# Kernel optimization log

Hardware: AMD Instinct MI355X
Metric: run time of the kernel (lower is better)

Reference implementation:

```python
import jax, jax.numpy as jnp
import numpy as np

H = 512; L = 2; V = 128; B = 128; T = 256; LW = 32; SOS = 1


def _lstm_scan(xs, Wih, Whh, b, reverse=False):
    # xs: [B, T, in]; Wih: [in, 4H]; Whh: [H, 4H]; b: [4H]
    Bq, Hh = xs.shape[0], Whh.shape[0]
    h0 = jnp.zeros((Bq, Hh), xs.dtype)

    def step(carry, xt):
        h, c = carry
        i, f, g, o = jnp.split(xt @ Wih + h @ Whh + b, 4, axis=-1)
        c = jax.nn.sigmoid(f) * c + jax.nn.sigmoid(i) * jnp.tanh(g)
        h = jax.nn.sigmoid(o) * jnp.tanh(c)
        return (h, c), h

    (hT, cT), ys = jax.lax.scan(step, (h0, h0), jnp.swapaxes(xs, 0, 1), reverse=reverse)
    return jnp.swapaxes(ys, 0, 1), hT, cT


def setup_inputs() -> dict:
    key = jax.random.key(0)
    ks = jax.random.split(key, 17)
    s = 0.05
    rn = lambda k, shape: jax.random.normal(k, shape, jnp.float32) * s
    return {
        'x': jax.random.normal(ks[0], (B, T, 2), jnp.float32),
        'enc_l0_Wih': rn(ks[1], (2, 2, 4 * H)),
        'enc_l0_Whh': rn(ks[2], (2, H, 4 * H)),
        'enc_l0_b': rn(ks[3], (2, 4 * H)),
        'enc_l1_Wih': rn(ks[4], (2, 2 * H, 4 * H)),
        'enc_l1_Whh': rn(ks[5], (2, H, 4 * H)),
        'enc_l1_b': rn(ks[6], (2, 4 * H)),
        'dec_Wih': rn(ks[7], (L, H, 4 * H)),
        'dec_Whh': rn(ks[8], (L, H, 4 * H)),
        'dec_b': rn(ks[9], (L, 4 * H)),
        'emb': rn(ks[10], (V, H)),
        'Wq': rn(ks[11], (H, 2 * H)),
        'bq': rn(ks[12], (2 * H,)),
        'Wc': rn(ks[13], (3 * H, H)),
        'bc': rn(ks[14], (H,)),
        'Wf': rn(ks[15], (H, V)),
        'bf': rn(ks[16], (V,)),
    }


def _forward(x, enc_l0_Wih, enc_l0_Whh, enc_l0_b, enc_l1_Wih, enc_l1_Whh, enc_l1_b,
             dec_Wih, dec_Whh, dec_b, emb, Wq, bq, Wc, bc, Wf, bf):
    # --- encoder: 2-layer bidirectional LSTM ---
    hs, cs = [], []
    inp = x
    for (Wih, Whh, b) in ((enc_l0_Wih, enc_l0_Whh, enc_l0_b),
                          (enc_l1_Wih, enc_l1_Whh, enc_l1_b)):
        yf, hf, cf = _lstm_scan(inp, Wih[0], Whh[0], b[0], reverse=False)
        yb, hb, cb = _lstm_scan(inp, Wih[1], Whh[1], b[1], reverse=True)
        inp = jnp.concatenate([yf, yb], axis=-1)
        hs.append(hf + hb)  # sum fwd+bwd final states (as in original)
        cs.append(cf + cb)
    enc_outs = inp                     # [B, T, 2H]
    h0 = jnp.stack(hs)                 # [L, B, H]
    c0 = jnp.stack(cs)
    tok0 = jnp.full((x.shape[0],), SOS, jnp.int32)

    def dec_step(carry, _):
        h, c, tok = carry
        layer_in = emb[tok]            # [B, H]
        nh, nc = [], []
        for l in range(L):
            i, f, g, o = jnp.split(layer_in @ dec_Wih[l] + h[l] @ dec_Whh[l] + dec_b[l], 4, axis=-1)
            cl = jax.nn.sigmoid(f) * c[l] + jax.nn.sigmoid(i) * jnp.tanh(g)
            hl = jax.nn.sigmoid(o) * jnp.tanh(cl)
            nh.append(hl); nc.append(cl)
            layer_in = hl
        dec_out = layer_in             # [B, H]
        query = dec_out @ Wq + bq      # [B, 2H]
        attn = jax.nn.softmax(jnp.einsum('bte,be->bt', enc_outs, query), axis=1)  # [B, T]
        context = jnp.einsum('bt,bte->be', attn, enc_outs)                        # [B, 2H]
        combined = jnp.concatenate([dec_out, context], axis=-1) @ Wc + bc         # [B, H]
        logits = combined @ Wf + bf                                                # [B, V]
        tok = jnp.argmax(logits, axis=-1).astype(jnp.int32)
        return (jnp.stack(nh), jnp.stack(nc), tok), (logits, attn)

    (hF, cF, _), (logits_seq, attn_seq) = jax.lax.scan(dec_step, (h0, c0, tok0), None, length=LW)
    output_seq = jnp.swapaxes(logits_seq, 0, 1)        # [B, LW, V]
    attention = jnp.transpose(attn_seq, (1, 2, 0))     # [B, T, LW]
    return output_seq, hF, cF, attention


def reference(x, enc_l0_Wih, enc_l0_Whh, enc_l0_b, enc_l1_Wih, enc_l1_Whh, enc_l1_b,
              dec_Wih, dec_Whh, dec_b, emb, Wq, bq, Wc, bc, Wf, bf):
    return _forward(x, enc_l0_Wih, enc_l0_Whh, enc_l0_b, enc_l1_Wih, enc_l1_Whh, enc_l1_b,
                    dec_Wih, dec_Whh, dec_b, emb, Wq, bq, Wc, bc, Wf, bf)
```

## Files before the change

kernel.cpp:

```cpp
#include <hip/hip_runtime.h>
#include <hip/hip_fp16.h>
#include <hip/hip_cooperative_groups.h>
#include <math.h>

#define NB 128
#define NT 256
#define NH 512
#define NG 2048
#define NV 128
#define NLW 32

__device__ __forceinline__ float sigf(float x){ return 1.0f/(1.0f + expf(-x)); }
__device__ __forceinline__ void fma4(float4& a, float s, float4 w){
  a.x += s*w.x; a.y += s*w.y; a.z += s*w.z; a.w += s*w.w;
}
__device__ __forceinline__ float4 ldh4(const __half* p){
  const __half2* p2 = (const __half2*)p;
  const float2 a = __half22float2(p2[0]);
  const float2 b = __half22float2(p2[1]);
  return make_float4(a.x, a.y, b.x, b.y);
}
__device__ __forceinline__ void ldh8(const __half* p, float4& lo, float4& hi){
  const float4 raw = *(const float4*)p;
  const __half2* h2 = (const __half2*)&raw;
  const float2 a = __half22float2(h2[0]);
  const float2 b = __half22float2(h2[1]);
  const float2 c = __half22float2(h2[2]);
  const float2 d = __half22float2(h2[3]);
  lo = make_float4(a.x, a.y, b.x, b.y);
  hi = make_float4(c.x, c.y, d.x, d.y);
}
__device__ __forceinline__ void dot4(float& acc, const float4 a, const float4 b){
  acc += a.x*b.x + a.y*b.y + a.z*b.z + a.w*b.w;
}

__device__ __forceinline__ void stc_f(float* p, float v){
  union { float f; unsigned u; } c; c.f = v;
  __hip_atomic_store((unsigned*)p, c.u, __ATOMIC_RELAXED, __HIP_MEMORY_SCOPE_AGENT);
}
__device__ __forceinline__ void stc_i(int* p, int v){
  __hip_atomic_store(p, v, __ATOMIC_RELAXED, __HIP_MEMORY_SCOPE_AGENT);
}

#define FBAR_FLAG0 1088
#define DBAR_FLAG0 1024

__device__ __forceinline__ void full_core(int* bar, int step) {
  const int g = blockIdx.x >> 4;
  const int prev = __hip_atomic_fetch_add(&bar[g*64], 1,
                     __ATOMIC_RELAXED, __HIP_MEMORY_SCOPE_AGENT);
  if (prev == 15) {
    const int r = __hip_atomic_fetch_add(&bar[16*64], 1,
                     __ATOMIC_RELAXED, __HIP_MEMORY_SCOPE_AGENT);
    if (r == 15) {
      #pragma unroll
      for (int i = 0; i < 16; ++i)
        __hip_atomic_store(&bar[i*64], 0, __ATOMIC_RELAXED, __HIP_MEMORY_SCOPE_AGENT);
      __hip_atomic_store(&bar[16*64], 0, __ATOMIC_RELAXED, __HIP_MEMORY_SCOPE_AGENT);
      asm volatile("s_waitcnt vmcnt(0)" ::: "memory");
      #pragma unroll 8
      for (int i = 0; i < 256; ++i)
        __hip_atomic_store(&bar[FBAR_FLAG0 + i*32], step,
                           __ATOMIC_RELAXED, __HIP_MEMORY_SCOPE_AGENT);
    }
  }
}
__device__ __forceinline__ void full_arrive(int* bar, int step) {
  __syncthreads();
  if (threadIdx.x == 0) {
    asm volatile("s_waitcnt vmcnt(0)" ::: "memory");
    full_core(bar, step);
  }
}
__device__ __forceinline__ void full_arrive_f(int* bar, int step) {
  __syncthreads();
  if (threadIdx.x == 0) {
    __threadfence();
    full_core(bar, step);
  }
}
__device__ __forceinline__ void full_wait(int* bar, int step) {
  if (threadIdx.x == 0) {
    int* my = &bar[FBAR_FLAG0 + blockIdx.x*32];
    while (__hip_atomic_load(my, __ATOMIC_RELAXED,
                             __HIP_MEMORY_SCOPE_AGENT) < step)
      __builtin_amdgcn_s_sleep(2);
    __threadfence();
  }
  __syncthreads();
}

__device__ __forceinline__ void dir_arrive(int* dbar, int step) {
  __syncthreads();
  if (threadIdx.x == 0) {
    asm volatile("s_waitcnt vmcnt(0)" ::: "memory");
    const int l = blockIdx.x & 127;
    const int g = l >> 4;
    const int prev = __hip_atomic_fetch_add(&dbar[g*64], 1,
                       __ATOMIC_RELAXED, __HIP_MEMORY_SCOPE_AGENT);
    if (prev == 15) {
      const int r = __hip_atomic_fetch_add(&dbar[8*64], 1,
                       __ATOMIC_RELAXED, __HIP_MEMORY_SCOPE_AGENT);
      if (r == 7) {
        #pragma unroll
        for (int i = 0; i < 8; ++i)
          __hip_atomic_store(&dbar[i*64], 0, __ATOMIC_RELAXED, __HIP_MEMORY_SCOPE_AGENT);
        __hip_atomic_store(&dbar[8*64], 0, __ATOMIC_RELAXED, __HIP_MEMORY_SCOPE_AGENT);
        asm volatile("s_waitcnt vmcnt(0)" ::: "memory");
        #pragma unroll 8
        for (int i = 0; i < 128; ++i)
          __hip_atomic_store(&dbar[DBAR_FLAG0 + i*32], step,
                             __ATOMIC_RELAXED, __HIP_MEMORY_SCOPE_AGENT);
      }
    }
  }
}
__device__ __forceinline__ void dir_wait(int* dbar, int step) {
  if (threadIdx.x == 0) {
    int* my = &dbar[DBAR_FLAG0 + (blockIdx.x & 127)*32];
    while (__hip_atomic_load(my, __ATOMIC_RELAXED,
                             __HIP_MEMORY_SCOPE_AGENT) < step)
      __builtin_amdgcn_s_sleep(2);
    __threadfence();
  }
  __syncthreads();
}

struct EncParams {
  const float* x;
  const float* W0ih; const float* W0hh; const float* b0;
  const float* W1ih; const float* W1hh; const float* b1;
  __half* y0; __half* enc;
  float* h0buf; float* h1buf;
  float* c0fin; float* c1fin;
  int*   bar;
};

#define W1T_ROW 1542
#define W0T_ROW 518
#define ENC_LDS_FLOATS (16*W1T_ROW + 16*W0T_ROW + 16 + 16 + 128*17)
#define ENC_LDS_BYTES  (ENC_LDS_FLOATS*4)

__device__ __forceinline__ void l1_ih_part(const __half* y0t, const float* W1T,
                                           const float* bias1, int bg2, int cg2,
                                           float acc[2][4]) {
  #pragma unroll
  for (int i = 0; i < 2; ++i)
    #pragma unroll
    for (int j = 0; j < 4; ++j)
      acc[i][j] = bias1[cg2*4 + j];
  const long r0 = (long)(bg2*2+0)*1024, r1 = (long)(bg2*2+1)*1024;
  #pragma unroll 2
  for (int k = 0; k < 1024; k += 8) {
    float4 a0lo, a0hi, a1lo, a1hi;
    ldh8(y0t + r0 + k, a0lo, a0hi);
    ldh8(y0t + r1 + k, a1lo, a1hi);
    #pragma unroll
    for (int j = 0; j < 4; ++j) {
      const float4 wlo = *(const float4*)&W1T[(cg2*4+j)*W1T_ROW + k];
      const float4 whi = *(const float4*)&W1T[(cg2*4+j)*W1T_ROW + k + 4];
      dot4(acc[0][j], a0lo, wlo); dot4(acc[0][j], a0hi, whi);
      dot4(acc[1][j], a1lo, wlo); dot4(acc[1][j], a1hi, whi);
    }
  }
}

__global__ __launch_bounds__(256, 1)
void encoder_kernel(EncParams P) {
  const int tid = threadIdx.x;
  const int bid = blockIdx.x;
  const int dir = bid >> 7;
  const int n0  = (bid & 127) * 4;
  int* dbar = P.bar + dir*8192;
  int* fbar = P.bar + 16384;

  extern __shared__ float lds[];
  float* W1T   = lds;
  float* W0T   = lds + 16*W1T_ROW;
  float* bias0 = W0T + 16*W0T_ROW;
  float* bias1 = bias0 + 16;
  float* gsm   = bias1 + 16;

  {
    const float* Wih1 = P.W1ih + (long)dir*1024*NG;
    const float* Whh1 = P.W1hh + (long)dir*512*NG;
    for (int e = tid; e < 16*1536; e += 256) {
      const int ci = e & 15, kk = e >> 4;
      const int gc = (ci>>2)*NH + n0 + (ci&3);
      W1T[ci*W1T_ROW + kk] = (kk < 1024) ? Wih1[(long)kk*NG + gc]
                                         : Whh1[(long)(kk-1024)*NG + gc];
    }
    const float* Wih0 = P.W0ih + (long)dir*2*NG;
    const float* Whh0 = P.W0hh + (long)dir*512*NG;
    for (int e = tid; e < 16*512; e += 256) {
      const int ci = e & 15, kk = e >> 4;
      const int gc = (ci>>2)*NH + n0 + (ci&3);
      W0T[ci*W0T_ROW + 4 + kk] = Whh0[(long)kk*NG + gc];
    }
    if (tid < 32) {
      const int ci = tid & 15, kk = tid >> 4;
      const int gc = (ci>>2)*NH + n0 + (ci&3);
      W0T[ci*W0T_ROW + kk] = Wih0[(long)kk*NG + gc];
    }
    if (tid < 16) {
      const int gc = (tid>>2)*NH + n0 + (tid&3);
      bias0[tid] = P.b0[(long)dir*NG + gc];
      bias1[tid] = P.b1[(long)dir*NG + gc];
    }
  }
  __syncthreads();

  int dstep = 0;
  float creg0 = 0.f, creg1 = 0.f;

  {
    const int bg1 = tid >> 3;
    const int cg1 = tid & 7;
    for (int p = 0; p < NT; ++p) {
      const int t = dir ? (NT-1 - p) : p;
      const float* hp = P.h0buf + (long)((p&1)*2 + dir)*65536;
      float acc[4][2];
      #pragma unroll
      for (int i = 0; i < 4; ++i) { acc[i][0] = bias0[cg1*2]; acc[i][1] = bias0[cg1*2+1]; }
      {
        const float w00 = W0T[(cg1*2+0)*W0T_ROW + 0], w01 = W0T[(cg1*2+0)*W0T_ROW + 1];
        const float w10 = W0T[(cg1*2+1)*W0T_ROW + 0], w11 = W0T[(cg1*2+1)*W0T_ROW + 1];
        #pragma unroll
        for (int i = 0; i < 4; ++i) {
          const int b = bg1*4 + i;
          const float x0 = P.x[(long)b*(NT*2) + t*2 + 0];
          const float x1 = P.x[(long)b*(NT*2) + t*2 + 1];
          acc[i][0] += x0*w00 + x1*w01;
          acc[i][1] += x0*w10 + x1*w11;
        }
      }
      #pragma unroll 4
      for (int k = 0; k < NH; k += 4) {
        const float4 w0 = *(const float4*)&W0T[(cg1*2+0)*W0T_ROW + 4 + k];
        const float4 w1 = *(const float4*)&W0T[(cg1*2+1)*W0T_ROW + 4 + k];
        #pragma unroll
        for (int i = 0; i < 4; ++i) {
          const float4 a = *(const float4*)&hp[(long)(bg1*4+i)*NH + k];
          dot4(acc[i][0], a, w0);
          dot4(acc[i][1], a, w1);
        }
      }
      #pragma unroll
      for (int i = 0; i < 4; ++i) {
        gsm[(bg1*4+i)*17 + cg1*2 + 0] = acc[i][0];
        gsm[(bg1*4+i)*17 + cg1*2 + 1] = acc[i][1];
      }
      __syncthreads();
      {
        float* hnext = P.h0buf + (long)(((p+1)&1)*2 + dir)*65536;
        #pragma unroll
        for (int r = 0; r < 2; ++r) {
          const int pi2 = tid + r*256;
          const int b = pi2 >> 2, nl = pi2 & 3;
          const float iv = gsm[b*17 + 0  + nl];
          const float fv = gsm[b*17 + 4  + nl];
          const float gv = gsm[b*17 + 8  + nl];
          const float ov = gsm[b*17 + 12 + nl];
          float cold = r ? creg1 : creg0;
          const float cn = sigf(fv)*cold + sigf(iv)*tanhf(gv);
          const float hn = sigf(ov)*tanhf(cn);
          if (r) creg1 = cn; else creg0 = cn;
          stc_f(&hnext[(long)b*NH + n0 + nl], hn);
          P.y0[((long)t*NB + b)*1024 + dir*NH + n0 + nl] = __float2half_rn(hn);
        }
      }
      if (p < NT-1) { ++dstep; dir_arrive(dbar, dstep); dir_wait(dbar, dstep); }
      else          { full_arrive_f(fbar, 1); full_wait(fbar, 1); }
    }
    #pragma unroll
    for (int r = 0; r < 2; ++r) {
      const int pi2 = tid + r*256;
      P.c0fin[(long)dir*65536 + (long)(pi2>>2)*NH + n0 + (pi2&3)] = r ? creg1 : creg0;
    }
    creg0 = 0.f; creg1 = 0.f;
  }

  {
    const int bg2 = tid >> 2;
    const int cg2 = tid & 3;
    float accN[2][4], accC[2][4];
    {
      const int t0i = dir ? (NT-1) : 0;
      l1_ih_part(P.y0 + (long)t0i*NB*1024, W1T, bias1, bg2, cg2, accN);
    }
    for (int p = 0; p < NT; ++p) {
      const int t = dir ? (NT-1 - p) : p;
      #pragma unroll
      for (int i = 0; i < 2; ++i)
        #pragma unroll
        for (int j = 0; j < 4; ++j)
          accC[i][j] = accN[i][j];
      {
        const float* hp = P.h1buf + (long)((p&1)*2 + dir)*65536;
        const long r0 = (long)(bg2*2+0)*NH, r1 = (long)(bg2*2+1)*NH;
        #pragma unroll 4
        for (int k = 0; k < NH; k += 4) {
          const float4 w0 = *(const float4*)&W1T[(cg2*4+0)*W1T_ROW + 1024 + k];
          const float4 w1 = *(const float4*)&W1T[(cg2*4+1)*W1T_ROW + 1024 + k];
          const float4 w2 = *(const float4*)&W1T[(cg2*4+2)*W1T_ROW + 1024 + k];
          const float4 w3 = *(const float4*)&W1T[(cg2*4+3)*W1T_ROW + 1024 + k];
          const float4 a0 = *(const float4*)&hp[r0 + k];
          const float4 a1 = *(const float4*)&hp[r1 + k];
          dot4(accC[0][0], a0, w0); dot4(accC[0][1], a0, w1);
          dot4(accC[0][2], a0, w2); dot4(accC[0][3], a0, w3);
          dot4(accC[1][0], a1, w0); dot4(accC[1][1], a1, w1);
          dot4(accC[1][2], a1, w2); dot4(accC[1][3], a1, w3);
        }
      }
      #pragma unroll
      for (int i = 0; i < 2; ++i)
        #pragma unroll
        for (int j = 0; j < 4; ++j)
          gsm[(bg2*2+i)*17 + cg2*4 + j] = accC[i][j];
      __syncthreads();
      {
        float* hnext = P.h1buf + (long)(((p+1)&1)*2 + dir)*65536;
        #pragma unroll
        for (int r = 0; r < 2; ++r) {
          const int pi2 = tid + r*256;
          const int b = pi2 >> 2, nl = pi2 & 3;
          const float iv = gsm[b*17 + 0  + nl];
          const float fv = gsm[b*17 + 4  + nl];
          const float gv = gsm[b*17 + 8  + nl];
          const float ov = gsm[b*17 + 12 + nl];
          float cold = r ? creg1 : creg0;
          const float cn = sigf(fv)*cold + sigf(iv)*tanhf(gv);
          const float hn = sigf(ov)*tanhf(cn);
          if (r) creg1 = cn; else creg0 = cn;
          stc_f(&hnext[(long)b*NH + n0 + nl], hn);
          P.enc[((long)t*NB + b)*1024 + dir*NH + n0 + nl] = __float2half_rn(hn);
        }
      }
      if (p < NT-1) {
        ++dstep; dir_arrive(dbar, dstep);
        const int tn = dir ? (NT-1 - (p+1)) : (p+1);
        l1_ih_part(P.y0 + (long)tn*NB*1024, W1T, bias1, bg2, cg2, accN);
        dir_wait(dbar, dstep);
      }
    }
    #pragma unroll
    for (int r = 0; r < 2; ++r) {
      const int pi2 = tid + r*256;
      P.c1fin[(long)dir*65536 + (long)(pi2>>2)*NH + n0 + (pi2&3)] = r ? creg1 : creg0;
    }
  }
}

struct DecParams {
  const float* emb;
  const float* dWih; const float* dWhh; const float* dbv;
  const float* Wq;  const float* bq;
  const float* Wc;  const float* bc;
  const float* Wf;  const float* bf;
  const __half* enc;
  const float* h0e; const float* h1e;
  const float* c0fin; const float* c1fin;
  float* dh0; float* dh1;
  float* query; float* ctx; float* comb;
  int*   tok;
  float* dout;
  int*   bar;
};

#define WD_ROW 1026
#define WQ_ROW 514
#define WC_ROW 1538
#define DEC_LDS_FLOATS (16*WD_ROW + 4*WQ_ROW + 2*WC_ROW + 16 + 4 + 2 + 128*17 \
                        + 1024 + 256 + 64 + 4 + 512 + 128 + 128)
#define DEC_LDS_BYTES  (DEC_LDS_FLOATS*4)

__global__ __launch_bounds__(256, 1)
void decoder_kernel(DecParams P) {
  const int tid = threadIdx.x;
  const int lid = blockIdx.x;
  const int L   = lid >> 7;
  const int n0  = (lid & 127) * 4;
  const int qc0 = lid * 4;
  const int cc0 = lid * 2;
  int* bar = P.bar;

  extern __shared__ float lds[];
  float* WD    = lds;
  float* WqT   = WD + 16*WD_ROW;
  float* WcT   = WqT + 4*WQ_ROW;
  float* biasD = WcT + 2*WC_ROW;
  float* bq4   = biasD + 16;
  float* bc2   = bq4 + 4;
  float* gsm   = bc2 + 2;
  float* qs    = gsm + 128*17;
  float* sc    = qs + 1024;
  float* ps    = sc + 256;
  float* m3    = ps + 64;
  float* cs    = m3 + 4;
  float* vals  = cs + 512;
  int*   idxs  = (int*)(vals + 128);

  {
    const float* Wih = P.dWih + (long)L*512*NG;
    const float* Whh = P.dWhh + (long)L*512*NG;
    for (int e = tid; e < 16*1024; e += 256) {
      const int ci = e & 15, kk = e >> 4;
      const int gc = (ci>>2)*NH + n0 + (ci&3);
      WD[ci*WD_ROW + kk] = (kk < 512) ? Wih[(long)kk*NG + gc]
                                      : Whh[(long)(kk-512)*NG + gc];
    }
    for (int e = tid; e < 4*512; e += 256) {
      const int c = e & 3, kk = e >> 2;
      WqT[c*WQ_ROW + kk] = P.Wq[(long)kk*1024 + qc0 + c];
    }
    for (int e = tid; e < 2*1536; e += 256) {
      const int c = e & 1, kk = e >> 1;
      WcT[c*WC_ROW + kk] = P.Wc[(long)kk*NH + cc0 + c];
    }
    if (tid < 16) biasD[tid] = P.dbv[(long)L*NG + (tid>>2)*NH + n0 + (tid&3)];
    if (tid < 4)  bq4[tid] = P.bq[qc0 + tid];
    if (tid < 2)  bc2[tid] = P.bc[cc0 + tid];
    const int i = lid*256 + tid;
    stc_f(&P.dh0[i], P.h0e[i] + P.h0e[65536 + i]);
    stc_f(&P.dh1[i], P.h1e[i] + P.h1e[65536 + i]);
    if (i < NB) stc_i(&P.tok[i], 1);
  }
  float cregA, cregB;
  {
    const float* cf = L ? P.c1fin : P.c0fin;
    const int b0i = tid >> 2, nl0 = tid & 3;
    cregA = cf[(long)b0i*NH + n0 + nl0] + cf[65536 + (long)b0i*NH + n0 + nl0];
    const int pi2 = tid + 256;
    const int b1i = pi2 >> 2, nl1 = pi2 & 3;
    cregB = cf[(long)b1i*NH + n0 + nl1] + cf[65536 + (long)b1i*NH + n0 + nl1];
  }
  int gstep = 0;
  ++gstep; full_arrive(bar, gstep); full_wait(bar, gstep);

  const int bg = tid >> 3;
  const int cg = tid & 7;

  for (int s = 0; s < NLW; ++s) {
    float* dh0c = P.dh0 + (s&1)*65536;
    float* dh0n = P.dh0 + ((s+1)&1)*65536;
    float* dh1c = P.dh1 + (s&1)*65536;
    float* dh1n = P.dh1 + ((s+1)&1)*65536;

    if (L == 0) {
      float acc[4][2];
      #pragma unroll
      for (int i = 0; i < 4; ++i) { acc[i][0] = biasD[cg*2]; acc[i][1] = biasD[cg*2+1]; }
      int rows[4];
      #pragma unroll
      for (int i = 0; i < 4; ++i) rows[i] = P.tok[bg*4 + i];
      #pragma unroll 4
      for (int k = 0; k < NH; k += 4) {
        const float4 w0 = *(const float4*)&WD[(cg*2+0)*WD_ROW + k];
        const float4 w1 = *(const float4*)&WD[(cg*2+1)*WD_ROW + k];
        #pragma unroll
        for (int i = 0; i < 4; ++i) {
          const float4 a = *(const float4*)&P.emb[(long)rows[i]*NH + k];
          dot4(acc[i][0], a, w0);
          dot4(acc[i][1], a, w1);
        }
      }
      #pragma unroll 4
      for (int k = 0; k < NH; k += 4) {
        const float4 w0 = *(const float4*)&WD[(cg*2+0)*WD_ROW + 512 + k];
        const float4 w1 = *(const float4*)&WD[(cg*2+1)*WD_ROW + 512 + k];
        #pragma unroll
        for (int i = 0; i < 4; ++i) {
          const float4 a = *(const float4*)&dh0c[(long)(bg*4+i)*NH + k];
          dot4(acc[i][0], a, w0);
          dot4(acc[i][1], a, w1);
        }
      }
      #pragma unroll
      for (int i = 0; i < 4; ++i) {
        gsm[(bg*4+i)*17 + cg*2 + 0] = acc[i][0];
        gsm[(bg*4+i)*17 + cg*2 + 1] = acc[i][1];
      }
      __syncthreads();
      #pragma unroll
      for (int r = 0; r < 2; ++r) {
        const int pi2 = tid + r*256;
        const int b = pi2 >> 2, nl = pi2 & 3;
        const float iv = gsm[b*17 + 0  + nl];
        const float fv = gsm[b*17 + 4  + nl];
        const float gv = gsm[b*17 + 8  + nl];
        const float ov = gsm[b*17 + 12 + nl];
        const float cold = r ? cregB : cregA;
        const float cn = sigf(fv)*cold + sigf(iv)*tanhf(gv);
        const float hn = sigf(ov)*tanhf(cn);
        if (r) cregB = cn; else cregA = cn;
        stc_f(&dh0n[(long)b*NH + n0 + nl], hn);
      }
    }
    ++gstep; full_arrive(bar, gstep); full_wait(bar, gstep);

    if (L == 1) {
      float acc[4][2];
      #pragma unroll
      for (int i = 0; i < 4; ++i) { acc[i][0] = biasD[cg*2]; acc[i][1] = biasD[cg*2+1]; }
      #pragma unroll 4
      for (int k = 0; k < NH; k += 4) {
        const float4 w0 = *(const float4*)&WD[(cg*2+0)*WD_ROW + k];
        const float4 w1 = *(const float4*)&WD[(cg*2+1)*WD_ROW + k];
        #pragma unroll
        for (int i = 0; i < 4; ++i) {
          const float4 a = *(const float4*)&dh0n[(long)(bg*4+i)*NH + k];
          dot4(acc[i][0], a, w0);
          dot4(acc[i][1], a, w1);
        }
      }
      #pragma unroll 4
      for (int k = 0; k < NH; k += 4) {
        const float4 w0 = *(const float4*)&WD[(cg*2+0)*WD_ROW + 512 + k];
        const float4 w1 = *(const float4*)&WD[(cg*2+1)*WD_ROW + 512 + k];
        #pragma unroll
        for (int i = 0; i < 4; ++i) {
          const float4 a = *(const float4*)&dh1c[(long)(bg*4+i)*NH + k];
          dot4(acc[i][0], a, w0);
          dot4(acc[i][1], a, w1);
        }
      }
      #pragma unroll
      for (int i = 0; i < 4; ++i) {
        gsm[(bg*4+i)*17 + cg*2 + 0] = acc[i][0];
        gsm[(bg*4+i)*17 + cg*2 + 1] = acc[i][1];
      }
      __syncthreads();
      #pragma unroll
      for (int r = 0; r < 2; ++r) {
        const int pi2 = tid + r*256;
        const int b = pi2 >> 2, nl = pi2 & 3;
        const float iv = gsm[b*17 + 0  + nl];
        const float fv = gsm[b*17 + 4  + nl];
        const float gv = gsm[b*17 + 8  + nl];
        const float ov = gsm[b*17 + 12 + nl];
        const float cold = r ? cregB : cregA;
        const float cn = sigf(fv)*cold + sigf(iv)*tanhf(gv);
        const float hn = sigf(ov)*tanhf(cn);
        if (r) cregB = cn; else cregA = cn;
        stc_f(&dh1n[(long)b*NH + n0 + nl], hn);
      }
    }
    ++gstep; full_arrive(bar, gstep); full_wait(bar, gstep);

    {
      const int b = tid >> 1;
      const int ch = (tid & 1) * 2;
      float a0 = bq4[ch + 0], a1 = bq4[ch + 1];
      const float* hr = dh1n + (long)b*NH;
      #pragma unroll 4
      for (int k = 0; k < NH; k += 4) {
        const float4 a = *(const float4*)&hr[k];
        const float4 w0 = *(const float4*)&WqT[(ch+0)*WQ_ROW + k];
        const float4 w1 = *(const float4*)&WqT[(ch+1)*WQ_ROW + k];
        dot4(a0, a, w0);
        dot4(a1, a, w1);
      }
      stc_f(&P.query[(long)b*1024 + qc0 + ch + 0], a0);
      stc_f(&P.query[(long)b*1024 + qc0 + ch + 1], a1);
    }
    ++gstep; full_arrive(bar, gstep); full_wait(bar, gstep);

    if (lid < NB) {
      const int b = lid;
      for (int i = tid; i < 1024; i += 256) qs[i] = P.query[(long)b*1024 + i];
      if (tid == 0) { m3[0] = -1e30f; m3[1] = 0.f; m3[2] = 0.f; }
      __syncthreads();
      float4 ctx4 = {0,0,0,0};
      for (int c = 0; c < 4; ++c) {
        const int t0 = c*64;
        {
          const int t_l = tid >> 2, part = tid & 3;
          const __half* er = P.enc + ((long)(t0 + t_l)*NB + b)*1024 + part*256;
          const float* qr = qs + part*256;
          float sv = 0.f;
          for (int k = 0; k < 256; k += 4) {
            const float4 e4 = ldh4(er + k);
            const float4 q4 = *(const float4*)(qr + k);
            sv += e4.x*q4.x + e4.y*q4.y + e4.z*q4.z + e4.w*q4.w;
          }
          sv += __shfl_xor(sv, 1);
          sv += __shfl_xor(sv, 2);
          if (part == 0) sc[t0 + t_l] = sv;
        }
        __syncthreads();
        if (tid < 64) {
          float sv = sc[t0 + tid];
          for (int off = 32; off; off >>= 1) sv = fmaxf(sv, __shfl_xor(sv, off));
          if (tid == 0) {
            const float mn = fmaxf(m3[0], sv);
            m3[2] = expf(m3[0] - mn);
            m3[0] = mn;
          }
        }
        __syncthreads();
        const float alpha = m3[2];
        if (tid < 64) {
          float pv = expf(sc[t0 + tid] - m3[0]);
          ps[tid] = pv;
          for (int off = 32; off; off >>= 1) pv += __shfl_xor(pv, off);
          if (tid == 0) m3[1] = m3[1]*alpha + pv;
        }
        __syncthreads();
        ctx4.x *= alpha; ctx4.y *= alpha; ctx4.z *= alpha; ctx4.w *= alpha;
        const __half* ecol = P.enc + ((long)t0*NB + b)*1024 + tid*4;
        for (int t = 0; t < 64; ++t) {
          const float4 e4 = ldh4(ecol + (long)t*(NB*1024));
          fma4(ctx4, ps[t], e4);
        }
        __syncthreads();
      }
      const float linv = 1.0f / m3[1];
      const long cb = (long)b*1024 + tid*4;
      stc_f(&P.ctx[cb+0], ctx4.x*linv); stc_f(&P.ctx[cb+1], ctx4.y*linv);
      stc_f(&P.ctx[cb+2], ctx4.z*linv); stc_f(&P.ctx[cb+3], ctx4.w*linv);
      const float pv = expf(sc[tid] - m3[0]) * linv;
      stc_f(&P.dout[786432L + (long)b*(NT*NLW) + (long)tid*NLW + s], pv);
    }
    ++gstep; full_arrive(bar, gstep); full_wait(bar, gstep);

    {
      const int b = tid >> 1;
      const int col = tid & 1;
      float acc = bc2[col];
      const float* hr = dh1n + (long)b*NH;
      #pragma unroll 4
      for (int k = 0; k < NH; k += 4) {
        const float4 a = *(const float4*)&hr[k];
        const float4 w = *(const float4*)&WcT[col*WC_ROW + k];
        dot4(acc, a, w);
      }
      const float* cr = P.ctx + (long)b*1024;
      #pragma unroll 4
      for (int k = 0; k < 1024; k += 4) {
        const float4 a = *(const float4*)&cr[k];
        const float4 w = *(const float4*)&WcT[col*WC_ROW + 512 + k];
        dot4(acc, a, w);
      }
      stc_f(&P.comb[(long)b*NH + cc0 + col], acc);
    }
    ++gstep; full_arrive(bar, gstep); full_wait(bar, gstep);

    if (lid < NB) {
      const int b = lid;
      for (int i = tid; i < NH; i += 256) cs[i] = P.comb[(long)b*NH + i];
      __syncthreads();
      if (tid < NV) {
        float acc = P.bf[tid];
        for (int k = 0; k < NH; k += 4) {
          const float4 c4 = *(const float4*)&cs[k];
          acc += c4.x*P.Wf[(long)(k+0)*NV + tid];
          acc += c4.y*P.Wf[(long)(k+1)*NV + tid];
          acc += c4.z*P.Wf[(long)(k+2)*NV + tid];
          acc += c4.w*P.Wf[(long)(k+3)*NV + tid];
        }
        stc_f(&P.dout[(long)b*(NLW*NV) + (long)s*NV + tid], acc);
        vals[tid] = acc; idxs[tid] = tid;
      }
      __syncthreads();
      for (int st = 64; st > 0; st >>= 1) {
        if (tid < st) {
          const float v2 = vals[tid+st]; const int i2 = idxs[tid+st];
          if (v2 > vals[tid] || (v2 == vals[tid] && i2 < idxs[tid])) { vals[tid] = v2; idxs[tid] = i2; }
        }
        __syncthreads();
      }
      if (tid == 0) stc_i(&P.tok[b], idxs[0]);
    }
    ++gstep; full_arrive(bar, gstep); full_wait(bar, gstep);
  }

  {
    const int i = lid*256 + tid;
    P.dout[524288L + i]         = P.dh0[i];
    P.dout[524288L + 65536 + i] = P.dh1[i];
    #pragma unroll
    for (int r = 0; r < 2; ++r) {
      const int pi2 = tid + r*256;
      const int b = pi2 >> 2, nl = pi2 & 3;
      P.dout[655360L + (long)L*65536 + (long)b*NH + n0 + nl] = r ? cregB : cregA;
    }
  }
}

struct StepDir {
  const void*  A;
  const float* WA;
  const float* Bs;
  const float* WB;
  const float* x2;
  const float* Wx;
  const int*   rowIdxA;
  const float* bias;
  float*  c_io;
  float*  h_out;
  __half* yh_out;
  int sA, KA, sB, KB, sx2, ystride, aHalf;
};
struct StepParams { StepDir d[2]; };

__global__ __launch_bounds__(256)
void lstm_step_kernel(StepParams P) {
  const StepDir p = P.d[blockIdx.z];
  const int tid = threadIdx.x;
  const int nq  = tid & 3;
  const int g   = (tid >> 2) & 3;
  const int bp  = tid >> 4;
  const int bl0 = bp*2;
  const int b0  = blockIdx.y*32 + bl0;
  const int n0  = blockIdx.x*16 + nq*4;
  const int gc  = g*NH + n0;

  float4 acc0 = *(const float4*)(p.bias + gc);
  float4 acc1 = acc0;

  if (p.x2) {
    const float4 w0 = *(const float4*)(p.Wx + gc);
    const float4 w1 = *(const float4*)(p.Wx + NG + gc);
    const float* xr0 = p.x2 + (long)b0     * p.sx2;
    const float* xr1 = p.x2 + (long)(b0+1) * p.sx2;
    fma4(acc0, xr0[0], w0); fma4(acc0, xr0[1], w1);
    fma4(acc1, xr1[0], w0); fma4(acc1, xr1[1], w1);
  }
  if (p.KA > 0) {
    const int r0 = p.rowIdxA ? p.rowIdxA[b0]   : b0;
    const int r1 = p.rowIdxA ? p.rowIdxA[b0+1] : b0+1;
    const float* Wp = p.WA + gc;
    if (p.aHalf) {
      const __half* rA0 = (const __half*)p.A + (long)r0 * p.sA;
      const __half* rA1 = (const __half*)p.A + (long)r1 * p.sA;
      for (int k = 0; k < p.KA; k += 4) {
        const float4 a0 = ldh4(rA0 + k);
        const float4 a1 = ldh4(rA1 + k);
        const float4 w0 = *(const float4*)(Wp + (long)(k+0)*NG);
        const float4 w1 = *(const float4*)(Wp + (long)(k+1)*NG);
        const float4 w2 = *(const float4*)(Wp + (long)(k+2)*NG);
        const float4 w3 = *(const float4*)(Wp + (long)(k+3)*NG);
        fma4(acc0, a0.x, w0); fma4(acc0, a0.y, w1); fma4(acc0, a0.z, w2); fma4(acc0, a0.w, w3);
        fma4(acc1, a1.x, w0); fma4(acc1, a1.y, w1); fma4(acc1, a1.z, w2); fma4(acc1, a1.w, w3);
      }
    } else {
      const float* rA0 = (const float*)p.A + (long)r0 * p.sA;
      const float* rA1 = (const float*)p.A + (long)r1 * p.sA;
      for (int k = 0; k < p.KA; k += 4) {
        const float4 a0 = *(const float4*)(rA0 + k);
        const float4 a1 = *(const float4*)(rA1 + k);
        const float4 w0 = *(const float4*)(Wp + (long)(k+0)*NG);
        const float4 w1 = *(const float4*)(Wp + (long)(k+1)*NG);
        const float4 w2 = *(const float4*)(Wp + (long)(k+2)*NG);
        const float4 w3 = *(const float4*)(Wp + (long)(k+3)*NG);
        fma4(acc0, a0.x, w0); fma4(acc0, a0.y, w1); fma4(acc0, a0.z, w2); fma4(acc0, a0.w, w3);
        fma4(acc1, a1.x, w0); fma4(acc1, a1.y, w1); fma4(acc1, a1.z, w2); fma4(acc1, a1.w, w3);
      }
    }
  }
  {
    const float* rB0 = p.Bs + (long)b0     * p.sB;
    const float* rB1 = p.Bs + (long)(b0+1) * p.sB;
    const float* Wp = p.WB + gc;
    for (int k = 0; k < p.KB; k += 4) {
      const float4 a0 = *(const float4*)(rB0 + k);
      const float4 a1 = *(const float4*)(rB1 + k);
      const float4 w0 = *(const float4*)(Wp + (long)(k+0)*NG);
      const float4 w1 = *(const float4*)(Wp + (long)(k+1)*NG);
      const float4 w2 = *(const float4*)(Wp + (long)(k+2)*NG);
      const float4 w3 = *(const float4*)(Wp + (long)(k+3)*NG);
      fma4(acc0, a0.x, w0); fma4(acc0, a0.y, w1); fma4(acc0, a0.z, w2); fma4(acc0, a0.w, w3);
      fma4(acc1, a1.x, w0); fma4(acc1, a1.y, w1); fma4(acc1, a1.z, w2); fma4(acc1, a1.w, w3);
    }
  }

  __shared__ __align__(16) float gs[32][68];
  {
    float* r0 = &gs[bl0][g*17 + nq*4];
    r0[0]=acc0.x; r0[1]=acc0.y; r0[2]=acc0.z; r0[3]=acc0.w;
    float* r1 = &gs[bl0+1][g*17 + nq*4];
    r1[0]=acc1.x; r1[1]=acc1.y; r1[2]=acc1.z; r1[3]=acc1.w;
  }
  __syncthreads();
  for (int pi = tid; pi < 512; pi += 256) {
    const int b_l = pi >> 4, n_l = pi & 15;
    const float iv = gs[b_l][0*17 + n_l];
    const float fv = gs[b_l][1*17 + n_l];
    const float gv = gs[b_l][2*17 + n_l];
    const float ov = gs[b_l][3*17 + n_l];
    const int bg = blockIdx.y*32 + b_l;
    const long idx = (long)bg*NH + blockIdx.x*16 + n_l;
    const float c_old = p.c_io[idx];
    const float cn = sigf(fv)*c_old + sigf(iv)*tanhf(gv);
    const float hn = sigf(ov)*tanhf(cn);
    p.c_io[idx]  = cn;
    p.h_out[idx] = hn;
    if (p.yh_out)
      p.yh_out[(long)bg*p.ystride + blockIdx.x*16 + n_l] = __float2half_rn(hn);
  }
}

struct LinParams {
  const float* A; const float* Bs; const float* W; const float* bias;
  float* out;
  int sA, KA, sB, KB, N;
};

__global__ __launch_bounds__(256)
void linear2_kernel(LinParams p) {
  __shared__ __align__(16) float As[64][36];
  const int tid = threadIdx.x;
  const int jl = tid & 63;
  const int j = blockIdx.x*64 + jl;
  const int bo = (tid >> 6)*8;
  const int bbase = blockIdx.y*32;
  float acc[8] = {0,0,0,0,0,0,0,0};
  for (int src = 0; src < 2; ++src) {
    const float* A = src ? p.Bs : p.A;
    const int sA   = src ? p.sB : p.sA;
    const int K    = src ? p.KB : p.KA;
    const float* W = src ? (p.W + (long)p.KA*p.N) : p.W;
    if (!A || K <= 0) continue;
    for (int k0 = 0; k0 < K; k0 += 64) {
      __syncthreads();
      for (int e = tid; e < 32*64; e += 256) {
        const int bl = e >> 6, kk = e & 63;
        As[kk][bl] = A[(long)(bbase+bl)*sA + k0 + kk];
      }
      __syncthreads();
      const float* Wp = W + (long)k0*p.N + j;
      for (int k = 0; k < 64; ++k) {
        const float wv = Wp[(long)k*p.N];
        const float4 aA = *(const float4*)&As[k][bo];
        const float4 aB = *(const float4*)&As[k][bo+4];
        acc[0] += aA.x*wv; acc[1] += aA.y*wv; acc[2] += aA.z*wv; acc[3] += aA.w*wv;
        acc[4] += aB.x*wv; acc[5] += aB.y*wv; acc[6] += aB.z*wv; acc[7] += aB.w*wv;
      }
    }
  }
  const float bv = p.bias ? p.bias[j] : 0.f;
  for (int i = 0; i < 8; ++i)
    p.out[(long)(bbase + bo + i)*p.N + j] = acc[i] + bv;
}

__global__ __launch_bounds__(256)
void attn_kernel(const float* __restrict__ query, const __half* __restrict__ enc,
                 float* __restrict__ context, float* __restrict__ attn_out, int step) {
  const int b = blockIdx.x;
  const int tid = threadIdx.x;
  __shared__ __align__(16) float qs[1024];
  __shared__ float sc[256];
  __shared__ float ps[64];
  __shared__ float msh, lsh, ash;
  for (int i = tid; i < 1024; i += 256) qs[i] = query[(long)b*1024 + i];
  if (tid == 0) { msh = -1e30f; lsh = 0.f; ash = 0.f; }
  __syncthreads();
  float4 ctx = {0,0,0,0};
  for (int c = 0; c < 4; ++c) {
    const int t0 = c*64;
    {
      const int t_l = tid >> 2, part = tid & 3;
      const __half* er = enc + ((long)(t0 + t_l)*NB + b)*1024 + part*256;
      const float* qr = qs + part*256;
      float sv = 0.f;
      for (int k = 0; k < 256; k += 4) {
        const float4 e4 = ldh4(er + k);
        const float4 q4 = *(const float4*)(qr + k);
        sv += e4.x*q4.x + e4.y*q4.y + e4.z*q4.z + e4.w*q4.w;
      }
      sv += __shfl_xor(sv, 1);
      sv += __shfl_xor(sv, 2);
      if (part == 0) sc[t0 + t_l] = sv;
    }
    __syncthreads();
    if (tid < 64) {
      float sv = sc[t0 + tid];
      for (int off = 32; off; off >>= 1) sv = fmaxf(sv, __shfl_xor(sv, off));
      if (tid == 0) {
        const float mn = fmaxf(msh, sv);
        ash = expf(msh - mn);
        msh = mn;
      }
    }
    __syncthreads();
    const float alpha = ash;
    if (tid < 64) {
      float pv = expf(sc[t0 + tid] - msh);
      ps[tid] = pv;
      for (int off = 32; off; off >>= 1) pv += __shfl_xor(pv, off);
      if (tid == 0) lsh = lsh*alpha + pv;
    }
    __syncthreads();
    ctx.x *= alpha; ctx.y *= alpha; ctx.z *= alpha; ctx.w *= alpha;
    const __half* ecol = enc + ((long)t0*NB + b)*1024 + tid*4;
    for (int t = 0; t < 64; ++t) {
      const float4 e4 = ldh4(ecol + (long)t*(NB*1024));
      fma4(ctx, ps[t], e4);
    }
    __syncthreads();
  }
  const float linv = 1.0f / lsh;
  const long cb = (long)b*1024 + tid*4;
  context[cb+0] = ctx.x*linv; context[cb+1] = ctx.y*linv;
  context[cb+2] = ctx.z*linv; context[cb+3] = ctx.w*linv;
  const float pv = expf(sc[tid] - msh) * linv;
  attn_out[(long)b*(NT*NLW) + (long)tid*NLW + step] = pv;
}

__global__ __launch_bounds__(128)
void logits_kernel(const float* __restrict__ comb, const float* __restrict__ Wf,
                   const float* __restrict__ bfv, float* __restrict__ out,
                   int sOut, int* __restrict__ tok) {
  const int b = blockIdx.x;
  const int v = threadIdx.x;
  __shared__ __align__(16) float cs[512];
  __shared__ float vals[128];
  __shared__ int idxs[128];
  for (int i = v; i < 512; i += 128) cs[i] = comb[(long)b*512 + i];
  __syncthreads();
  float acc = bfv[v];
  for (int k = 0; k < 512; k += 4) {
    const float4 c4 = *(const float4*)&cs[k];
    acc += c4.x*Wf[(long)(k+0)*NV + v];
    acc += c4.y*Wf[(long)(k+1)*NV + v];
    acc += c4.z*Wf[(long)(k+2)*NV + v];
    acc += c4.w*Wf[(long)(k+3)*NV + v];
  }
  out[(long)b*sOut + v] = acc;
  vals[v] = acc; idxs[v] = v;
  __syncthreads();
  for (int s = 64; s > 0; s >>= 1) {
    if (v < s) {
      const float v2 = vals[v+s]; const int i2 = idxs[v+s];
      if (v2 > vals[v] || (v2 == vals[v] && i2 < idxs[v])) { vals[v] = v2; idxs[v] = i2; }
    }
    __syncthreads();
  }
  if (v == 0) tok[b] = idxs[0];
}

__global__ void init_dec_kernel(const float* h00, const float* h01,
                                const float* c00, const float* c01,
                                const float* h10, const float* h11,
                                const float* c10, const float* c11,
                                float* dh0, float* dh1, float* dc0, float* dc1,
                                int* tok) {
  const int i = blockIdx.x*256 + threadIdx.x;
  dh0[i] = h00[i] + h01[i];
  dc0[i] = c00[i] + c01[i];
  dh1[i] = h10[i] + h11[i];
  dc1[i] = c10[i] + c11[i];
  if (i < NB) tok[i] = 1;
}

__global__ void final_copy_kernel(const float* dh0, const float* dh1,
                                  const float* dc0, const float* dc1,
                                  float* out_h, float* out_c) {
  const int i = blockIdx.x*256 + threadIdx.x;
  out_h[i] = dh0[i]; out_h[65536 + i] = dh1[i];
  out_c[i] = dc0[i]; out_c[65536 + i] = dc1[i];
}

extern "C" void kernel_launch(void* const* d_in, const int* in_sizes, int n_in,
                              void* d_out_v, int out_size, void* d_ws, size_t ws_size,
                              hipStream_t stream) {
  (void)in_sizes; (void)n_in; (void)out_size;
  const float* x    = (const float*)d_in[0];
  const float* W0ih = (const float*)d_in[1];
  const float* W0hh = (const float*)d_in[2];
  const float* b0v  = (const float*)d_in[3];
  const float* W1ih = (const float*)d_in[4];
  const float* W1hh = (const float*)d_in[5];
  const float* b1v  = (const float*)d_in[6];
  const float* dWih = (const float*)d_in[7];
  const float* dWhh = (const float*)d_in[8];
  const float* dbv  = (const float*)d_in[9];
  const float* emb  = (const float*)d_in[10];
  const float* Wq   = (const float*)d_in[11];
  const float* bq   = (const float*)d_in[12];
  const float* Wc   = (const float*)d_in[13];
  const float* bc   = (const float*)d_in[14];
  const float* Wf   = (const float*)d_in[15];
  const float* bfv  = (const float*)d_in[16];

  const long Y0_SLOTS  = 16777216L;
  const long ENC_SLOTS = 16777216L;
  const long BAR_SLOTS = 40960L;
  const long ST_SZ     = 786432L + BAR_SLOTS;
  const long DEC_SZ    = 655488L;
  const long NEEDED    = Y0_SLOTS + ENC_SLOTS + ST_SZ + DEC_SZ;
  if (ws_size < (size_t)NEEDED*4) return;

  float*  ws    = (float*)d_ws;
  __half* y0h   = (__half*)ws;
  __half* ench  = (__half*)(ws + Y0_SLOTS);
  float*  st    = ws + Y0_SLOTS + ENC_SLOTS;
  float*  h0buf = st;
  float*  h1buf = st + 262144;
  float*  c0fin = st + 524288;
  float*  c1fin = st + 655360;
  int*    barE  = (int*)(st + 786432);
  int*    barD  = barE + 28672;
  float*  dec   = st + ST_SZ;
  float* ddh0  = dec + 0;
  float* ddh1  = dec + 131072;
  float* dcomb = dec + 262144;
  float* query = dec + 393216;
  float* ctx   = dec + 524288;
  int*   tok   = (int*)(dec + 655360);
  float* dh[2][2] = {{dec+0, dec+65536}, {dec+131072, dec+196608}};
  float* dc[2]    =  {dec+262144, dec+327680};
  float* comb  = query;
  float* dout  = (float*)d_out_v;

  hipMemsetAsync(st, 0, ST_SZ*4, stream);

  EncParams EP;
  EP.x = x; EP.W0ih = W0ih; EP.W0hh = W0hh; EP.b0 = b0v;
  EP.W1ih = W1ih; EP.W1hh = W1hh; EP.b1 = b1v;
  EP.y0 = y0h; EP.enc = ench;
  EP.h0buf = h0buf; EP.h1buf = h1buf; EP.c0fin = c0fin; EP.c1fin = c1fin;
  EP.bar = barE;

  static int attrDone = 0;
  if (!attrDone) {
    (void)hipFuncSetAttribute(reinterpret_cast<const void*>(encoder_kernel),
                              hipFuncAttributeMaxDynamicSharedMemorySize,
                              ENC_LDS_BYTES);
    (void)hipFuncSetAttribute(reinterpret_cast<const void*>(decoder_kernel),
                              hipFuncAttributeMaxDynamicSharedMemorySize,
                              DEC_LDS_BYTES);
    attrDone = 1;
  }
  void* eargs[] = { (void*)&EP };
  hipError_t cerr = hipLaunchCooperativeKernel(
      reinterpret_cast<const void*>(encoder_kernel),
      dim3(256), dim3(256), eargs, (unsigned int)ENC_LDS_BYTES, stream);

  if (cerr != hipSuccess) {
    for (int p = 0; p < NT; ++p) {
      StepParams SP{};
      for (int d = 0; d < 2; ++d) {
        const int t = d ? (NT-1-p) : p;
        StepDir& q = SP.d[d];
        q.A = nullptr; q.WA = nullptr; q.sA = 0; q.KA = 0; q.aHalf = 0;
        q.Bs = h0buf + (long)((p&1)*2 + d)*65536; q.sB = NH; q.KB = NH;
        q.WB = W0hh + (long)d*NH*NG;
        q.x2 = x + (long)t*2; q.sx2 = NT*2; q.Wx = W0ih + (long)d*2*NG;
        q.rowIdxA = nullptr; q.bias = b0v + (long)d*NG;
        q.c_io = c0fin + (long)d*65536;
        q.h_out = h0buf + (long)(((p+1)&1)*2 + d)*65536;
        q.yh_out = y0h + (long)t*(NB*1024) + d*NH; q.ystride = 1024;
      }
      lstm_step_kernel<<<dim3(32,4,2), 256, 0, stream>>>(SP);
    }
    for (int p = 0; p < NT; ++p) {
      StepParams SP{};
      for (int d = 0; d < 2; ++d) {
        const int t = d ? (NT-1-p) : p;
        StepDir& q = SP.d[d];
        q.A = y0h + (long)t*(NB*1024); q.aHalf = 1; q.sA = 1024; q.KA = 2*NH;
        q.WA = W1ih + (long)d*(2*NH)*NG;
        q.Bs = h1buf + (long)((p&1)*2 + d)*65536; q.sB = NH; q.KB = NH;
        q.WB = W1hh + (long)d*NH*NG;
        q.x2 = nullptr; q.sx2 = 0; q.Wx = nullptr;
        q.rowIdxA = nullptr; q.bias = b1v + (long)d*NG;
        q.c_io = c1fin + (long)d*65536;
        q.h_out = h1buf + (long)(((p+1)&1)*2 + d)*65536;
        q.yh_out = ench + (long)t*(NB*1024) + d*NH; q.ystride = 1024;
      }
      lstm_step_kernel<<<dim3(32,4,2), 256, 0, stream>>>(SP);
    }
  }

  DecParams DP;
  DP.emb = emb; DP.dWih = dWih; DP.dWhh = dWhh; DP.dbv = dbv;
  DP.Wq = Wq; DP.bq = bq; DP.Wc = Wc; DP.bc = bc; DP.Wf = Wf; DP.bf = bfv;
  DP.enc = ench;
  DP.h0e = h0buf; DP.h1e = h1buf;
  DP.c0fin = c0fin; DP.c1fin = c1fin;
  DP.dh0 = ddh0; DP.dh1 = ddh1;
  DP.query = query; DP.ctx = ctx; DP.comb = dcomb;
  DP.tok = tok; DP.dout = dout; DP.bar = barD;

  void* dargs[] = { (void*)&DP };
  hipError_t derr = hipLaunchCooperativeKernel(
      reinterpret_cast<const void*>(decoder_kernel),
      dim3(256), dim3(256), dargs, (unsigned int)DEC_LDS_BYTES, stream);

  if (derr != hipSuccess) {
    init_dec_kernel<<<256, 256, 0, stream>>>(h0buf, h0buf+65536, c0fin, c0fin+65536,
                                             h1buf, h1buf+65536, c1fin, c1fin+65536,
                                             dh[0][0], dh[1][0], dc[0], dc[1], tok);
    for (int s = 0; s < NLW; ++s) {
      const int si = s&1, so = (s+1)&1;
      {
        StepParams SP{};
        StepDir& q = SP.d[0];
        q.A = emb; q.sA = NH; q.KA = NH; q.aHalf = 0; q.WA = dWih;
        q.Bs = dh[0][si]; q.sB = NH; q.KB = NH; q.WB = dWhh;
        q.x2 = nullptr; q.sx2 = 0; q.Wx = nullptr;
        q.rowIdxA = tok;
        q.bias = dbv;
        q.c_io = dc[0]; q.h_out = dh[0][so];
        q.yh_out = nullptr; q.ystride = 0;
        lstm_step_kernel<<<dim3(32,4,1), 256, 0, stream>>>(SP);
      }
      {
        StepParams SP{};
        StepDir& q = SP.d[0];
        q.A = dh[0][so]; q.sA = NH; q.KA = NH; q.aHalf = 0; q.WA = dWih + (long)NH*NG;
        q.Bs = dh[1][si]; q.sB = NH; q.KB = NH; q.WB = dWhh + (long)NH*NG;
        q.x2 = nullptr; q.sx2 = 0; q.Wx = nullptr;
        q.rowIdxA = nullptr;
        q.bias = dbv + NG;
        q.c_io = dc[1]; q.h_out = dh[1][so];
        q.yh_out = nullptr; q.ystride = 0;
        lstm_step_kernel<<<dim3(32,4,1), 256, 0, stream>>>(SP);
      }
      {
        LinParams LP{ dh[1][so], nullptr, Wq, bq, query, NH, NH, 0, 0, 2*NH };
        linear2_kernel<<<dim3(16,4), 256, 0, stream>>>(LP);
      }
      attn_kernel<<<128, 256, 0, stream>>>(query, ench, ctx, dout + 786432L, s);
      {
        LinParams LP{ dh[1][so], ctx, Wc, bc, comb, NH, NH, 2*NH, 2*NH, NH };
        linear2_kernel<<<dim3(8,4), 256, 0, stream>>>(LP);
      }
      logits_kernel<<<128, 128, 0, stream>>>(comb, Wf, bfv, dout + (long)s*NV,
                                             NLW*NV, tok);
    }
    final_copy_kernel<<<256, 256, 0, stream>>>(dh[0][0], dh[1][0], dc[0], dc[1],
                                               dout + 524288L, dout + 655360L);
  }
}
```

Baseline: 39.66 ms.

## Fuse decoder query, attention, combine and logits into one per-batch block phase

The query projection, context and combine projections no longer run spread across all blocks with a grid barrier between each. Each of the 128 batch blocks now computes its own query, attention, combined vector and logits locally, reading Wq and Wc straight from global memory. This removes three grid-wide barriers per decoder step and the global round-trips for query, ctx and comb. In exchange, the 128 blocks each re-read the full Wq and Wc matrices every step while the other 128 blocks sit idle, which adds L2 traffic and serial work per block.

```diff
diff --git a/kernel.cpp b/kernel.cpp
--- a/kernel.cpp
+++ b/kernel.cpp
@@ -368,10 +368,7 @@
 };
 
 #define WD_ROW 1026
-#define WQ_ROW 514
-#define WC_ROW 1538
-#define DEC_LDS_FLOATS (16*WD_ROW + 4*WQ_ROW + 2*WC_ROW + 16 + 4 + 2 + 128*17 \
-                        + 1024 + 256 + 64 + 4 + 512 + 128 + 128)
+#define DEC_LDS_FLOATS (16*WD_ROW + 16 + 128*17 + 1024 + 256 + 64 + 4 + 512 + 1024 + 128 + 128)
 #define DEC_LDS_BYTES  (DEC_LDS_FLOATS*4)
 
 __global__ __launch_bounds__(256, 1)
@@ -380,24 +377,19 @@
   const int lid = blockIdx.x;
   const int L   = lid >> 7;
   const int n0  = (lid & 127) * 4;
-  const int qc0 = lid * 4;
-  const int cc0 = lid * 2;
   int* bar = P.bar;
 
   extern __shared__ float lds[];
   float* WD    = lds;
-  float* WqT   = WD + 16*WD_ROW;
-  float* WcT   = WqT + 4*WQ_ROW;
-  float* biasD = WcT + 2*WC_ROW;
-  float* bq4   = biasD + 16;
-  float* bc2   = bq4 + 4;
-  float* gsm   = bc2 + 2;
+  float* biasD = WD + 16*WD_ROW;
+  float* gsm   = biasD + 16;
   float* qs    = gsm + 128*17;
   float* sc    = qs + 1024;
   float* ps    = sc + 256;
   float* m3    = ps + 64;
   float* cs    = m3 + 4;
-  float* vals  = cs + 512;
+  float* ctxs  = cs + 512;
+  float* vals  = ctxs + 1024;
   int*   idxs  = (int*)(vals + 128);
 
   {
@@ -409,17 +401,7 @@
       WD[ci*WD_ROW + kk] = (kk < 512) ? Wih[(long)kk*NG + gc]
                                       : Whh[(long)(kk-512)*NG + gc];
     }
-    for (int e = tid; e < 4*512; e += 256) {
-      const int c = e & 3, kk = e >> 2;
-      WqT[c*WQ_ROW + kk] = P.Wq[(long)kk*1024 + qc0 + c];
-    }
-    for (int e = tid; e < 2*1536; e += 256) {
-      const int c = e & 1, kk = e >> 1;
-      WcT[c*WC_ROW + kk] = P.Wc[(long)kk*NH + cc0 + c];
-    }
     if (tid < 16) biasD[tid] = P.dbv[(long)L*NG + (tid>>2)*NH + n0 + (tid&3)];
-    if (tid < 4)  bq4[tid] = P.bq[qc0 + tid];
-    if (tid < 2)  bc2[tid] = P.bc[cc0 + tid];
     const int i = lid*256 + tid;
     stc_f(&P.dh0[i], P.h0e[i] + P.h0e[65536 + i]);
     stc_f(&P.dh1[i], P.h1e[i] + P.h1e[65536 + i]);
@@ -547,28 +529,27 @@
     }
     ++gstep; full_arrive(bar, gstep); full_wait(bar, gstep);
 
-    {
-      const int b = tid >> 1;
-      const int ch = (tid & 1) * 2;
-      float a0 = bq4[ch + 0], a1 = bq4[ch + 1];
-      const float* hr = dh1n + (long)b*NH;
-      #pragma unroll 4
-      for (int k = 0; k < NH; k += 4) {
-        const float4 a = *(const float4*)&hr[k];
-        const float4 w0 = *(const float4*)&WqT[(ch+0)*WQ_ROW + k];
-        const float4 w1 = *(const float4*)&WqT[(ch+1)*WQ_ROW + k];
-        dot4(a0, a, w0);
-        dot4(a1, a, w1);
-      }
-      stc_f(&P.query[(long)b*1024 + qc0 + ch + 0], a0);
-      stc_f(&P.query[(long)b*1024 + qc0 + ch + 1], a1);
-    }
-    ++gstep; full_arrive(bar, gstep); full_wait(bar, gstep);
-
     if (lid < NB) {
       const int b = lid;
-      for (int i = tid; i < 1024; i += 256) qs[i] = P.query[(long)b*1024 + i];
+      for (int i = tid; i < NH; i += 256) cs[i] = dh1n[(long)b*NH + i];
       if (tid == 0) { m3[0] = -1e30f; m3[1] = 0.f; m3[2] = 0.f; }
+      __syncthreads();
+      {
+        const int jc = tid*4;
+        float4 a4 = *(const float4*)&P.bq[jc];
+        for (int k = 0; k < NH; k += 4) {
+          const float h0 = cs[k], h1 = cs[k+1], h2 = cs[k+2], h3 = cs[k+3];
+          const float4 r0 = *(const float4*)&P.Wq[(long)(k+0)*1024 + jc];
+          const float4 r1 = *(const float4*)&P.Wq[(long)(k+1)*1024 + jc];
+          const float4 r2 = *(const float4*)&P.Wq[(long)(k+2)*1024 + jc];
+          const float4 r3 = *(const float4*)&P.Wq[(long)(k+3)*1024 + jc];
+          a4.x += h0*r0.x + h1*r1.x + h2*r2.x + h3*r3.x;
+          a4.y += h0*r0.y + h1*r1.y + h2*r2.y + h3*r3.y;
+          a4.z += h0*r0.z + h1*r1.z + h2*r2.z + h3*r3.z;
+          a4.w += h0*r0.w + h1*r1.w + h2*r2.w + h3*r3.w;
+        }
+        *(float4*)&qs[jc] = a4;
+      }
       __syncthreads();
       float4 ctx4 = {0,0,0,0};
       for (int c = 0; c < 4; ++c) {
@@ -615,56 +596,53 @@
         __syncthreads();
       }
       const float linv = 1.0f / m3[1];
-      const long cb = (long)b*1024 + tid*4;
-      stc_f(&P.ctx[cb+0], ctx4.x*linv); stc_f(&P.ctx[cb+1], ctx4.y*linv);
-      stc_f(&P.ctx[cb+2], ctx4.z*linv); stc_f(&P.ctx[cb+3], ctx4.w*linv);
+      ctxs[tid*4+0] = ctx4.x*linv; ctxs[tid*4+1] = ctx4.y*linv;
+      ctxs[tid*4+2] = ctx4.z*linv; ctxs[tid*4+3] = ctx4.w*linv;
       const float pv = expf(sc[tid] - m3[0]) * linv;
-      stc_f(&P.dout[786432L + (long)b*(NT*NLW) + (long)tid*NLW + s], pv);
-    }
-    ++gstep; full_arrive(bar, gstep); full_wait(bar, gstep);
-
-    {
-      const int b = tid >> 1;
-      const int col = tid & 1;
-      float acc = bc2[col];
-      const float* hr = dh1n + (long)b*NH;
-      #pragma unroll 4
-      for (int k = 0; k < NH; k += 4) {
-        const float4 a = *(const float4*)&hr[k];
-        const float4 w = *(const float4*)&WcT[col*WC_ROW + k];
-        dot4(acc, a, w);
-      }
-      const float* cr = P.ctx + (long)b*1024;
-      #pragma unroll 4
-      for (int k = 0; k < 1024; k += 4) {
-        const float4 a = *(const float4*)&cr[k];
-        const float4 w = *(const float4*)&WcT[col*WC_ROW + 512 + k];
-        dot4(acc, a, w);
-      }
-      stc_f(&P.comb[(long)b*NH + cc0 + col], acc);
-    }
-    ++gstep; full_arrive(bar, gstep); full_wait(bar, gstep);
-
-    if (lid < NB) {
-      const int b = lid;
-      for (int i = tid; i < NH; i += 256) cs[i] = P.comb[(long)b*NH + i];
+      P.dout[786432L + (long)b*(NT*NLW) + (long)tid*NLW + s] = pv;
+      __syncthreads();
+      {
+        const int c2 = tid*2;
+        float ax = P.bc[c2 + 0], ay = P.bc[c2 + 1];
+        for (int k = 0; k < NH; k += 4) {
+          const float h0 = cs[k], h1 = cs[k+1], h2 = cs[k+2], h3 = cs[k+3];
+          const float2 r0 = *(const float2*)&P.Wc[(long)(k+0)*NH + c2];
+          const float2 r1 = *(const float2*)&P.Wc[(long)(k+1)*NH + c2];
+          const float2 r2 = *(const float2*)&P.Wc[(long)(k+2)*NH + c2];
+          const float2 r3 = *(const float2*)&P.Wc[(long)(k+3)*NH + c2];
+          ax += h0*r0.x + h1*r1.x + h2*r2.x + h3*r3.x;
+          ay += h0*r0.y + h1*r1.y + h2*r2.y + h3*r3.y;
+        }
+        for (int k = 0; k < 1024; k += 4) {
+          const float h0 = ctxs[k], h1 = ctxs[k+1], h2 = ctxs[k+2], h3 = ctxs[k+3];
+          const float2 r0 = *(const float2*)&P.Wc[(long)(512+k+0)*NH + c2];
+          const float2 r1 = *(const float2*)&P.Wc[(long)(512+k+1)*NH + c2];
+          const float2 r2 = *(const float2*)&P.Wc[(long)(512+k+2)*NH + c2];
+          const float2 r3 = *(const float2*)&P.Wc[(long)(512+k+3)*NH + c2];
+          ax += h0*r0.x + h1*r1.x + h2*r2.x + h3*r3.x;
+          ay += h0*r0.y + h1*r1.y + h2*r2.y + h3*r3.y;
+        }
+        __syncthreads();
+        qs[c2 + 0] = ax;
+        qs[c2 + 1] = ay;
+      }
       __syncthreads();
       if (tid < NV) {
         float acc = P.bf[tid];
         for (int k = 0; k < NH; k += 4) {
-          const float4 c4 = *(const float4*)&cs[k];
+          const float4 c4 = *(const float4*)&qs[k];
           acc += c4.x*P.Wf[(long)(k+0)*NV + tid];
           acc += c4.y*P.Wf[(long)(k+1)*NV + tid];
           acc += c4.z*P.Wf[(long)(k+2)*NV + tid];
           acc += c4.w*P.Wf[(long)(k+3)*NV + tid];
         }
-        stc_f(&P.dout[(long)b*(NLW*NV) + (long)s*NV + tid], acc);
+        P.dout[(long)b*(NLW*NV) + (long)s*NV + tid] = acc;
         vals[tid] = acc; idxs[tid] = tid;
       }
       __syncthreads();
-      for (int st = 64; st > 0; st >>= 1) {
-        if (tid < st) {
-          const float v2 = vals[tid+st]; const int i2 = idxs[tid+st];
+      for (int st2 = 64; st2 > 0; st2 >>= 1) {
+        if (tid < st2) {
+          const float v2 = vals[tid+st2]; const int i2 = idxs[tid+st2];
           if (v2 > vals[tid] || (v2 == vals[tid] && i2 < idxs[tid])) { vals[tid] = v2; idxs[tid] = i2; }
         }
         __syncthreads();
```

New measurement: 38.95 ms. No clear change (-1.8%).
